# Optimization experiments

Hardware: AMD Instinct MI355X
Metric: run time of the kernel (lower is better)

Reference implementation:

```python
import jax, jax.numpy as jnp
import numpy as np

V, P, D, H, HD, L, FF = 21128, 512, 768, 12, 64, 12, 3072
COEF = np.array([[1,1,0,0,0,0,0,0,0,0,0,1],[1,1,1,1,0,0,0,0,0,0,0,1],[1,1,1,1,1,1,0,0,0,0,0,1],[1,1,1,1,1,1,1,1,0,0,0,1],[1,1,1,1,1,1,1,1,1,1,0,1]], dtype=np.float32)

def _ln(x, g, b):
    mu = jnp.mean(x, -1, keepdims=True)
    v = jnp.mean((x - mu) ** 2, -1, keepdims=True)
    return (x - mu) / jnp.sqrt(v + 1e-12) * g + b

def _gelu(x):
    return x * 0.5 * (1.0 + jax.lax.erf(x * 0.7071067811865475))

def setup_inputs() -> dict:
    key = jax.random.key(0)
    ks = jax.random.split(key, 16)
    B, S, LE = 16, 512, 256
    input_ids = jax.random.randint(ks[0], (B, S), 0, V)
    mask = jnp.ones((B, S), jnp.float32)
    epid = jax.random.randint(ks[1], (B, LE), 0, 10)
    epid = epid.at[:, -1].set(9)  # ensure encoder_turn=9 -> coefficient row 4
    s = 0.02
    def nrm(k, shape):
        return jax.random.normal(k, shape, jnp.float32) * s
    return {
        'input_ids': input_ids, 'mask': mask, 'encoder_position_id': epid,
        'word_emb': nrm(ks[2], (V, D)), 'pos_emb': nrm(ks[3], (P, D)),
        'emb_ln_g': jnp.ones((D,)), 'emb_ln_b': jnp.zeros((D,)),
        'Wq': nrm(ks[4], (L, D, D)), 'bq': jnp.zeros((L, D)),
        'Wk': nrm(ks[5], (L, D, D)), 'bk': jnp.zeros((L, D)),
        'Wv': nrm(ks[6], (L, D, D)), 'bv': jnp.zeros((L, D)),
        'Wo': nrm(ks[7], (L, D, D)), 'bo': jnp.zeros((L, D)),
        'ln1_g': jnp.ones((L, D)), 'ln1_b': jnp.zeros((L, D)),
        'Wi': nrm(ks[8], (L, D, FF)), 'bi': jnp.zeros((L, FF)),
        'Wo2': nrm(ks[9], (L, FF, D)), 'bo2': jnp.zeros((L, D)),
        'ln2_g': jnp.ones((L, D)), 'ln2_b': jnp.zeros((L, D)),
        'coef': jnp.tile(jnp.asarray(COEF)[None], (L, 1, 1)),
    }

def reference(input_ids, mask, encoder_position_id, word_emb, pos_emb, emb_ln_g, emb_ln_b,
              Wq, bq, Wk, bk, Wv, bv, Wo, bo, ln1_g, ln1_b, Wi, bi, Wo2, bo2, ln2_g, ln2_b, coef):
    B, S = input_ids.shape
    LE = encoder_position_id.shape[1]
    # causal+padding mask: floor((m+m^T)/2) on {0,1} == AND == product, then tril
    am = jnp.tril(mask[:, None, None, :] * mask[:, None, :, None])  # [B,1,S,S]
    # position coefficient machinery
    turn = jnp.max(encoder_position_id, -1)           # [B]
    row = ((turn - 1) // 2).astype(jnp.int32)         # row into [5,12] table
    enc_pm = jax.nn.one_hot(encoder_position_id, 12, dtype=jnp.float32)  # [B,LE,12]
    dec_pm = jnp.zeros((B, S - LE, 12), jnp.float32).at[:, :, 11].set(1.0)
    pm = jnp.concatenate([enc_pm, dec_pm], 1)         # [B,S,12]
    # embeddings (token_type not used in forward; past_length=0)
    h = _ln(word_emb[input_ids] + pos_emb[jnp.arange(S)], emb_ln_g, emb_ln_b)
    for l in range(L):
        coef_row = coef[l][row]                       # [B,12]
        ps = jnp.einsum('bsk,bk->bs', pm, coef_row)   # per-key modulation [B,S]
        q = (h @ Wq[l] + bq[l]).reshape(B, S, H, HD)
        k = (h @ Wk[l] + bk[l]).reshape(B, S, H, HD)
        v = (h @ Wv[l] + bv[l]).reshape(B, S, H, HD)
        scores = jnp.einsum('bqhd,bkhd->bhqk', q, k) / 8.0
        scores = scores * ps[:, None, None, :]
        scores = scores * am - 1e10 * (1.0 - am)
        probs = jax.nn.softmax(scores, -1)
        ctx = jnp.einsum('bhqk,bkhd->bqhd', probs, v).reshape(B, S, D)
        a = _ln(ctx @ Wo[l] + bo[l] + h, ln1_g[l], ln1_b[l])
        ff = _gelu(a @ Wi[l] + bi[l])
        h = _ln(ff @ Wo2[l] + bo2[l] + a, ln2_g[l], ln2_b[l])
    return h
```

## Files before the change

kernel.cpp:

```cpp
#include <hip/hip_runtime.h>

#define SEQ 512
#define NB  16
#define DIM 768
#define NH  12
#define HDIM 64
#define NL  12
#define FFD 3072
#define MTOK 8192

typedef _Float16 half8 __attribute__((ext_vector_type(8)));
typedef float    floatx4 __attribute__((ext_vector_type(4)));

__device__ __forceinline__ void load_lds16(const void* g, void* l) {
  __builtin_amdgcn_global_load_lds((__attribute__((address_space(1))) void*)g,
                                   (__attribute__((address_space(3))) void*)l, 16, 0, 0);
}

__device__ __forceinline__ float blockSum768(float v) {
  __shared__ float red[4];
  #pragma unroll
  for (int d = 32; d; d >>= 1) v += __shfl_xor(v, d);
  const int wv = threadIdx.x >> 6;
  __syncthreads();
  if ((threadIdx.x & 63) == 0) red[wv] = v;
  __syncthreads();
  return red[0] + red[1] + red[2] + red[3];
}

__device__ __forceinline__ void ln_store(float x0, float x1, float x2,
                                         const float* __restrict__ g,
                                         const float* __restrict__ bb,
                                         float* __restrict__ yf,
                                         _Float16* __restrict__ yh, int row) {
  const int tid = threadIdx.x;
  const float mu = blockSum768(x0 + x1 + x2) * (1.0f / 768.0f);
  const float d0 = x0 - mu, d1 = x1 - mu, d2 = x2 - mu;
  const float var = blockSum768(d0 * d0 + d1 * d1 + d2 * d2) * (1.0f / 768.0f);
  const float inv = rsqrtf(var + 1e-12f);
  const size_t base = (size_t)row * DIM;
  const float y0 = d0 * inv * g[tid]       + bb[tid];
  const float y1 = d1 * inv * g[tid + 256] + bb[tid + 256];
  const float y2 = d2 * inv * g[tid + 512] + bb[tid + 512];
  if (yf) { yf[base + tid] = y0; yf[base + tid + 256] = y1; yf[base + tid + 512] = y2; }
  yh[base + tid] = (_Float16)y0; yh[base + tid + 256] = (_Float16)y1; yh[base + tid + 512] = (_Float16)y2;
}

__global__ __launch_bounds__(256) void embed_ln_k(const int* __restrict__ ids,
                                                  const float* __restrict__ we,
                                                  const float* __restrict__ pe,
                                                  const float* __restrict__ g,
                                                  const float* __restrict__ bb,
                                                  float* __restrict__ hf,
                                                  _Float16* __restrict__ hh) {
  const int tok = blockIdx.x;
  const int s = tok & (SEQ - 1);
  const int id = ids[tok];
  const int tid = threadIdx.x;
  float x[3];
  #pragma unroll
  for (int j = 0; j < 3; ++j) {
    const int d = tid + j * 256;
    x[j] = we[(size_t)id * DIM + d] + pe[(size_t)s * DIM + d];
  }
  ln_store(x[0], x[1], x[2], g, bb, hf, hh, tok);
}

__global__ __launch_bounds__(256) void ln_k(const float* __restrict__ xin,
                                            const float* __restrict__ g,
                                            const float* __restrict__ bb,
                                            float* __restrict__ yf,
                                            _Float16* __restrict__ yh) {
  const int row = blockIdx.x;
  const int tid = threadIdx.x;
  float x[3];
  #pragma unroll
  for (int j = 0; j < 3; ++j) x[j] = xin[(size_t)row * DIM + tid + j * 256];
  ln_store(x[0], x[1], x[2], g, bb, yf, yh, row);
}

__global__ __launch_bounds__(256) void transpose_k(const float* __restrict__ in,
                                                   _Float16* __restrict__ out,
                                                   int K, int N) {
  __shared__ float tile[32][33];
  const int z = blockIdx.z;
  in  += (size_t)z * K * N;
  out += (size_t)z * K * N;
  const int n0 = blockIdx.x * 32, k0 = blockIdx.y * 32;
  const int tx = threadIdx.x & 31, ty = threadIdx.x >> 5;
  #pragma unroll
  for (int i = 0; i < 32; i += 8) tile[ty + i][tx] = in[(size_t)(k0 + ty + i) * N + n0 + tx];
  __syncthreads();
  #pragma unroll
  for (int i = 0; i < 32; i += 8) out[(size_t)(n0 + ty + i) * K + k0 + tx] = (_Float16)tile[tx][ty + i];
}

__global__ __launch_bounds__(512) void ps_k(const int* __restrict__ epid,
                                            const float* __restrict__ coef,
                                            float* __restrict__ ps_all) {
  __shared__ int red[8];
  const int b = blockIdx.x, tid = threadIdx.x;
  int e = (tid < 256) ? epid[b * 256 + tid] : 0;
  #pragma unroll
  for (int d = 32; d; d >>= 1) e = max(e, __shfl_xor(e, d));
  if ((tid & 63) == 0) red[tid >> 6] = e;
  __syncthreads();
  int turn = red[0];
  #pragma unroll
  for (int i = 1; i < 8; ++i) turn = max(turn, red[i]);
  int row = (turn - 1) >> 1;
  row = max(0, min(4, row));
  const int pe = (tid < 256) ? epid[b * 256 + tid] : 11;
  #pragma unroll
  for (int l = 0; l < NL; ++l)
    ps_all[((size_t)l * NB + b) * SEQ + tid] = coef[(l * 5 + row) * 12 + pe];
}

template <bool RES, bool GELU, bool WF, bool WH>
__global__ __launch_bounds__(256) void gemm_f16(const _Float16* __restrict__ A,
                                                const _Float16* __restrict__ Bt,
                                                const float* __restrict__ bias,
                                                const float* __restrict__ resid,
                                                float* __restrict__ outF,
                                                _Float16* __restrict__ outH,
                                                int M, int N, int K) {
  __shared__ __align__(16) _Float16 Als[128 * 32];
  __shared__ __align__(16) _Float16 Bls[128 * 32];
  const int tid = threadIdx.x, lane = tid & 63, wave = tid >> 6;
  const int bm0 = blockIdx.y * 128, bn0 = blockIdx.x * 128;
  const int lr = lane & 15, lk = lane >> 4;
  const int wm = (wave >> 1) * 64, wn = (wave & 1) * 64;
  floatx4 acc[4][4] = {};

  const int srow = lane >> 2;
  const int scol = (lane & 3) * 8;
  const _Float16* Ag = A  + (size_t)(bm0 + wave * 16 + srow) * K + scol;
  const _Float16* Bg = Bt + (size_t)(bn0 + wave * 16 + srow) * K + scol;
  _Float16* Al = &Als[wave * 16 * 32];
  _Float16* Bl = &Bls[wave * 16 * 32];
  const size_t rs64 = (size_t)64 * K;

  for (int kt = 0; kt < K; kt += 32) {
    load_lds16(Ag + kt,        Al);
    load_lds16(Ag + rs64 + kt, Al + 64 * 32);
    load_lds16(Bg + kt,        Bl);
    load_lds16(Bg + rs64 + kt, Bl + 64 * 32);
    __syncthreads();
    half8 af[4], bf[4];
    #pragma unroll
    for (int i = 0; i < 4; ++i) {
      af[i] = *(const half8*)&Als[(wm + i * 16 + lr) * 32 + lk * 8];
      bf[i] = *(const half8*)&Bls[(wn + i * 16 + lr) * 32 + lk * 8];
    }
    #pragma unroll
    for (int mi = 0; mi < 4; ++mi)
      #pragma unroll
      for (int ni = 0; ni < 4; ++ni)
        acc[mi][ni] = __builtin_amdgcn_mfma_f32_16x16x32_f16(af[mi], bf[ni], acc[mi][ni], 0, 0, 0);
    __syncthreads();
  }

  #pragma unroll
  for (int mi = 0; mi < 4; ++mi) {
    #pragma unroll
    for (int r = 0; r < 4; ++r) {
      const int row = bm0 + wm + mi * 16 + lk * 4 + r;
      const size_t ro = (size_t)row * N;
      #pragma unroll
      for (int ni = 0; ni < 4; ++ni) {
        const int col = bn0 + wn + ni * 16 + lr;
        float x = acc[mi][ni][r] + bias[col];
        if (RES)  x += resid[ro + col];
        if (GELU) x = 0.5f * x * (1.0f + erff(x * 0.70710678118654752f));
        if (WF) outF[ro + col] = x;
        if (WH) outH[ro + col] = (_Float16)x;
      }
    }
  }
}

__global__ __launch_bounds__(256) void attn_k(const _Float16* __restrict__ q,
                                              const _Float16* __restrict__ k,
                                              const _Float16* __restrict__ v,
                                              const float* __restrict__ ps,
                                              const float* __restrict__ mask,
                                              _Float16* __restrict__ ctx) {
  __shared__ __align__(16) _Float16 kls[64 * 64];
  __shared__ __align__(16) _Float16 vtls[64 * 64];
  __shared__ __align__(16) _Float16 pls[4][32 * 64];
  const int tid = threadIdx.x, lane = tid & 63, wave = tid >> 6;
  const int qt = blockIdx.x, h = blockIdx.y, b = blockIdx.z;
  const int lr = lane & 15, lk = lane >> 4;
  const int q0 = qt * 128 + wave * 32;

  half8 qf[2][2];
  #pragma unroll
  for (int mi = 0; mi < 2; ++mi)
    #pragma unroll
    for (int ks = 0; ks < 2; ++ks)
      qf[mi][ks] = *(const half8*)&q[(size_t)(b * SEQ + q0 + mi * 16 + lr) * DIM + h * HDIM + ks * 32 + lk * 8];

  floatx4 o[2][4] = {};
  float m_run[2][4], l_run[2][4], mq[2][4];
  #pragma unroll
  for (int mi = 0; mi < 2; ++mi)
    #pragma unroll
    for (int r = 0; r < 4; ++r) {
      m_run[mi][r] = -3e38f; l_run[mi][r] = 0.f;
      mq[mi][r] = mask[b * SEQ + q0 + mi * 16 + lk * 4 + r];
    }

  const int nt = 2 * (qt + 1);
  for (int t = 0; t < nt; ++t) {
    const int kb = t * 64;
    #pragma unroll
    for (int i = 0; i < 2; ++i) {
      const int idx = tid + i * 256;
      const int key = idx >> 3, c8 = (idx & 7) * 8;
      const size_t gkv = (size_t)(b * SEQ + kb + key) * DIM + h * HDIM + c8;
      *(half8*)&kls[key * 64 + c8] = *(const half8*)&k[gkv];
      half8 vv = *(const half8*)&v[gkv];
      #pragma unroll
      for (int j = 0; j < 8; ++j) vtls[(c8 + j) * 64 + key] = vv[j];
    }
    __syncthreads();

    floatx4 s[2][4] = {};
    #pragma unroll
    for (int ks = 0; ks < 2; ++ks)
      #pragma unroll
      for (int ni = 0; ni < 4; ++ni) {
        half8 kf = *(const half8*)&kls[(ni * 16 + lr) * 64 + ks * 32 + lk * 8];
        #pragma unroll
        for (int mi = 0; mi < 2; ++mi)
          s[mi][ni] = __builtin_amdgcn_mfma_f32_16x16x32_f16(qf[mi][ks], kf, s[mi][ni], 0, 0, 0);
      }

    float pk[4], km[4]; int kidx[4];
    #pragma unroll
    for (int ni = 0; ni < 4; ++ni) {
      kidx[ni] = kb + ni * 16 + lr;
      pk[ni] = ps[b * SEQ + kidx[ni]] * 0.125f;
      km[ni] = mask[b * SEQ + kidx[ni]];
    }

    #pragma unroll
    for (int mi = 0; mi < 2; ++mi) {
      #pragma unroll
      for (int r = 0; r < 4; ++r) {
        const int rq = q0 + mi * 16 + lk * 4 + r;
        float sc[4]; float mt = -3e38f;
        #pragma unroll
        for (int ni = 0; ni < 4; ++ni) {
          const float am = (kidx[ni] <= rq) ? km[ni] * mq[mi][r] : 0.f;
          const float x = s[mi][ni][r] * pk[ni] * am - 1e10f * (1.f - am);
          sc[ni] = x; mt = fmaxf(mt, x);
        }
        #pragma unroll
        for (int d = 1; d < 16; d <<= 1) mt = fmaxf(mt, __shfl_xor(mt, d));
        const float mnew = fmaxf(m_run[mi][r], mt);
        const float corr = __expf(m_run[mi][r] - mnew);
        float rsum = 0.f;
        #pragma unroll
        for (int ni = 0; ni < 4; ++ni) {
          const float p = __expf(sc[ni] - mnew);
          rsum += p;
          pls[wave][(mi * 16 + lk * 4 + r) * 64 + ni * 16 + lr] = (_Float16)p;
        }
        #pragma unroll
        for (int d = 1; d < 16; d <<= 1) rsum += __shfl_xor(rsum, d);
        l_run[mi][r] = l_run[mi][r] * corr + rsum;
        m_run[mi][r] = mnew;
        #pragma unroll
        for (int ni = 0; ni < 4; ++ni) o[mi][ni][r] *= corr;
      }
    }

    #pragma unroll
    for (int mi = 0; mi < 2; ++mi) {
      half8 pf[2];
      #pragma unroll
      for (int ks = 0; ks < 2; ++ks)
        pf[ks] = *(const half8*)&pls[wave][(mi * 16 + lr) * 64 + ks * 32 + lk * 8];
      #pragma unroll
      for (int ni = 0; ni < 4; ++ni)
        #pragma unroll
        for (int ks = 0; ks < 2; ++ks)
          o[mi][ni] = __builtin_amdgcn_mfma_f32_16x16x32_f16(
              pf[ks], *(const half8*)&vtls[(ni * 16 + lr) * 64 + ks * 32 + lk * 8], o[mi][ni], 0, 0, 0);
    }
    __syncthreads();
  }

  #pragma unroll
  for (int mi = 0; mi < 2; ++mi)
    #pragma unroll
    for (int r = 0; r < 4; ++r) {
      const float inv = 1.f / l_run[mi][r];
      const int rq = q0 + mi * 16 + lk * 4 + r;
      #pragma unroll
      for (int ni = 0; ni < 4; ++ni)
        ctx[(size_t)(b * SEQ + rq) * DIM + h * HDIM + ni * 16 + lr] = (_Float16)(o[mi][ni][r] * inv);
    }
}

extern "C" void kernel_launch(void* const* d_in, const int* in_sizes, int n_in,
                              void* d_out, int out_size, void* d_ws, size_t ws_size,
                              hipStream_t stream) {
  const int*   ids  = (const int*)d_in[0];
  const float* mask = (const float*)d_in[1];
  const int*   epid = (const int*)d_in[2];
  const float* we   = (const float*)d_in[3];
  const float* pe   = (const float*)d_in[4];
  const float* elng = (const float*)d_in[5];
  const float* elnb = (const float*)d_in[6];
  const float* Wq   = (const float*)d_in[7];  const float* bq  = (const float*)d_in[8];
  const float* Wk   = (const float*)d_in[9];  const float* bk  = (const float*)d_in[10];
  const float* Wv   = (const float*)d_in[11]; const float* bv  = (const float*)d_in[12];
  const float* Wo   = (const float*)d_in[13]; const float* bo  = (const float*)d_in[14];
  const float* ln1g = (const float*)d_in[15]; const float* ln1b = (const float*)d_in[16];
  const float* Wi   = (const float*)d_in[17]; const float* bi  = (const float*)d_in[18];
  const float* Wo2  = (const float*)d_in[19]; const float* bo2 = (const float*)d_in[20];
  const float* ln2g = (const float*)d_in[21]; const float* ln2b = (const float*)d_in[22];
  const float* coef = (const float*)d_in[23];
  float* out = (float*)d_out;

  char* w = (char*)d_ws;
  auto alloc = [&](size_t bytes) { char* p = w; w += (bytes + 255) & ~(size_t)255; return p; };
  const size_t WSM = (size_t)DIM * DIM;
  const size_t WLG = (size_t)DIM * FFD;
  _Float16* wqT  = (_Float16*)alloc(NL * WSM * 2);
  _Float16* wkT  = (_Float16*)alloc(NL * WSM * 2);
  _Float16* wvT  = (_Float16*)alloc(NL * WSM * 2);
  _Float16* woT  = (_Float16*)alloc(NL * WSM * 2);
  _Float16* wiT  = (_Float16*)alloc(NL * WLG * 2);
  _Float16* wo2T = (_Float16*)alloc(NL * WLG * 2);
  float*    h_f32 = (float*)alloc((size_t)MTOK * DIM * 4);
  _Float16* h_f16 = (_Float16*)alloc((size_t)MTOK * DIM * 2);
  float*    a_f32 = (float*)alloc((size_t)MTOK * DIM * 4);
  _Float16* a_f16 = (_Float16*)alloc((size_t)MTOK * DIM * 2);
  float*    tmp   = (float*)alloc((size_t)MTOK * DIM * 4);
  _Float16* q_f16 = (_Float16*)alloc((size_t)MTOK * DIM * 2);
  _Float16* k_f16 = (_Float16*)alloc((size_t)MTOK * DIM * 2);
  _Float16* v_f16 = (_Float16*)alloc((size_t)MTOK * DIM * 2);
  _Float16* c_f16 = (_Float16*)alloc((size_t)MTOK * DIM * 2);
  _Float16* ff_f16 = (_Float16*)alloc((size_t)MTOK * FFD * 2);
  float*    ps_all = (float*)alloc((size_t)NL * NB * SEQ * 4);

  transpose_k<<<dim3(24, 24, NL), 256, 0, stream>>>(Wq,  wqT,  DIM, DIM);
  transpose_k<<<dim3(24, 24, NL), 256, 0, stream>>>(Wk,  wkT,  DIM, DIM);
  transpose_k<<<dim3(24, 24, NL), 256, 0, stream>>>(Wv,  wvT,  DIM, DIM);
  transpose_k<<<dim3(24, 24, NL), 256, 0, stream>>>(Wo,  woT,  DIM, DIM);
  transpose_k<<<dim3(96, 24, NL), 256, 0, stream>>>(Wi,  wiT,  DIM, FFD);
  transpose_k<<<dim3(24, 96, NL), 256, 0, stream>>>(Wo2, wo2T, FFD, DIM);
  ps_k<<<NB, 512, 0, stream>>>(epid, coef, ps_all);
  embed_ln_k<<<MTOK, 256, 0, stream>>>(ids, we, pe, elng, elnb, h_f32, h_f16);

  for (int l = 0; l < NL; ++l) {
    gemm_f16<false, false, false, true><<<dim3(6, 64), 256, 0, stream>>>(
        h_f16, wqT + (size_t)l * WSM, bq + l * DIM, nullptr, nullptr, q_f16, MTOK, DIM, DIM);
    gemm_f16<false, false, false, true><<<dim3(6, 64), 256, 0, stream>>>(
        h_f16, wkT + (size_t)l * WSM, bk + l * DIM, nullptr, nullptr, k_f16, MTOK, DIM, DIM);
    gemm_f16<false, false, false, true><<<dim3(6, 64), 256, 0, stream>>>(
        h_f16, wvT + (size_t)l * WSM, bv + l * DIM, nullptr, nullptr, v_f16, MTOK, DIM, DIM);
    attn_k<<<dim3(4, NH, NB), 256, 0, stream>>>(
        q_f16, k_f16, v_f16, ps_all + (size_t)l * NB * SEQ, mask, c_f16);
    gemm_f16<true, false, true, false><<<dim3(6, 64), 256, 0, stream>>>(
        c_f16, woT + (size_t)l * WSM, bo + l * DIM, h_f32, tmp, nullptr, MTOK, DIM, DIM);
    ln_k<<<MTOK, 256, 0, stream>>>(tmp, ln1g + l * DIM, ln1b + l * DIM, a_f32, a_f16);
    gemm_f16<false, true, false, true><<<dim3(24, 64), 256, 0, stream>>>(
        a_f16, wiT + (size_t)l * WLG, bi + l * FFD, nullptr, nullptr, ff_f16, MTOK, FFD, DIM);
    gemm_f16<true, false, true, false><<<dim3(6, 64), 256, 0, stream>>>(
        ff_f16, wo2T + (size_t)l * WLG, bo2 + l * DIM, a_f32, tmp, nullptr, MTOK, DIM, FFD);
    ln_k<<<MTOK, 256, 0, stream>>>(tmp, ln2g + l * DIM, ln2b + l * DIM,
                                   (l == NL - 1) ? out : h_f32, h_f16);
  }
}
```

Before: 5.075 ms.

## Fuse QKV projections into one GEMM and swizzle attention LDS tiles

```diff
diff --git a/kernel.cpp b/kernel.cpp
--- a/kernel.cpp
+++ b/kernel.cpp
@@ -8,6 +8,7 @@
 #define NL  12
 #define FFD 3072
 #define MTOK 8192
+#define QKVD 2304
 
 typedef _Float16 half8 __attribute__((ext_vector_type(8)));
 typedef float    floatx4 __attribute__((ext_vector_type(4)));
@@ -81,11 +82,11 @@
 
 __global__ __launch_bounds__(256) void transpose_k(const float* __restrict__ in,
                                                    _Float16* __restrict__ out,
-                                                   int K, int N) {
+                                                   int K, int N, size_t ozs) {
   __shared__ float tile[32][33];
   const int z = blockIdx.z;
   in  += (size_t)z * K * N;
-  out += (size_t)z * K * N;
+  out += (size_t)z * ozs;
   const int n0 = blockIdx.x * 32, k0 = blockIdx.y * 32;
   const int tx = threadIdx.x & 31, ty = threadIdx.x >> 5;
   #pragma unroll
@@ -93,6 +94,18 @@
   __syncthreads();
   #pragma unroll
   for (int i = 0; i < 32; i += 8) out[(size_t)(n0 + ty + i) * K + k0 + tx] = (_Float16)tile[tx][ty + i];
+}
+
+__global__ __launch_bounds__(256) void concat_bias_k(const float* __restrict__ bq,
+                                                     const float* __restrict__ bk,
+                                                     const float* __restrict__ bv,
+                                                     float* __restrict__ dst) {
+  const int l = blockIdx.x;
+  for (int j = threadIdx.x; j < DIM; j += 256) {
+    dst[(size_t)l * QKVD + j]           = bq[l * DIM + j];
+    dst[(size_t)l * QKVD + DIM + j]     = bk[l * DIM + j];
+    dst[(size_t)l * QKVD + 2 * DIM + j] = bv[l * DIM + j];
+  }
 }
 
 __global__ __launch_bounds__(512) void ps_k(const int* __restrict__ epid,
@@ -179,9 +192,7 @@
   }
 }
 
-__global__ __launch_bounds__(256) void attn_k(const _Float16* __restrict__ q,
-                                              const _Float16* __restrict__ k,
-                                              const _Float16* __restrict__ v,
+__global__ __launch_bounds__(256) void attn_k(const _Float16* __restrict__ qkv,
                                               const float* __restrict__ ps,
                                               const float* __restrict__ mask,
                                               _Float16* __restrict__ ctx) {
@@ -189,7 +200,8 @@
   __shared__ __align__(16) _Float16 vtls[64 * 64];
   __shared__ __align__(16) _Float16 pls[4][32 * 64];
   const int tid = threadIdx.x, lane = tid & 63, wave = tid >> 6;
-  const int qt = blockIdx.x, h = blockIdx.y, b = blockIdx.z;
+  const int qt = 3 - blockIdx.x;
+  const int h = blockIdx.y, b = blockIdx.z;
   const int lr = lane & 15, lk = lane >> 4;
   const int q0 = qt * 128 + wave * 32;
 
@@ -198,7 +210,7 @@
   for (int mi = 0; mi < 2; ++mi)
     #pragma unroll
     for (int ks = 0; ks < 2; ++ks)
-      qf[mi][ks] = *(const half8*)&q[(size_t)(b * SEQ + q0 + mi * 16 + lr) * DIM + h * HDIM + ks * 32 + lk * 8];
+      qf[mi][ks] = *(const half8*)&qkv[(size_t)(b * SEQ + q0 + mi * 16 + lr) * QKVD + h * HDIM + ks * 32 + lk * 8];
 
   floatx4 o[2][4] = {};
   float m_run[2][4], l_run[2][4], mq[2][4];
@@ -210,6 +222,7 @@
       mq[mi][r] = mask[b * SEQ + q0 + mi * 16 + lk * 4 + r];
     }
 
+  const int swzA = (lr & 7) * 8;
   const int nt = 2 * (qt + 1);
   for (int t = 0; t < nt; ++t) {
     const int kb = t * 64;
@@ -217,11 +230,15 @@
     for (int i = 0; i < 2; ++i) {
       const int idx = tid + i * 256;
       const int key = idx >> 3, c8 = (idx & 7) * 8;
-      const size_t gkv = (size_t)(b * SEQ + kb + key) * DIM + h * HDIM + c8;
-      *(half8*)&kls[key * 64 + c8] = *(const half8*)&k[gkv];
-      half8 vv = *(const half8*)&v[gkv];
-      #pragma unroll
-      for (int j = 0; j < 8; ++j) vtls[(c8 + j) * 64 + key] = vv[j];
+      *(half8*)&kls[key * 64 + (c8 ^ ((key & 7) * 8))] =
+          *(const half8*)&qkv[(size_t)(b * SEQ + kb + key) * QKVD + DIM + h * HDIM + c8];
+      const int keyv = idx & 63, c8v = (idx >> 6) * 8;
+      half8 vv = *(const half8*)&qkv[(size_t)(b * SEQ + kb + keyv) * QKVD + 2 * DIM + h * HDIM + c8v];
+      #pragma unroll
+      for (int j = 0; j < 8; ++j) {
+        const int d = c8v + j;
+        vtls[d * 64 + (keyv ^ ((d & 7) * 8))] = vv[j];
+      }
     }
     __syncthreads();
 
@@ -230,7 +247,7 @@
     for (int ks = 0; ks < 2; ++ks)
       #pragma unroll
       for (int ni = 0; ni < 4; ++ni) {
-        half8 kf = *(const half8*)&kls[(ni * 16 + lr) * 64 + ks * 32 + lk * 8];
+        half8 kf = *(const half8*)&kls[(ni * 16 + lr) * 64 + ((ks * 32 + lk * 8) ^ swzA)];
         #pragma unroll
         for (int mi = 0; mi < 2; ++mi)
           s[mi][ni] = __builtin_amdgcn_mfma_f32_16x16x32_f16(qf[mi][ks], kf, s[mi][ni], 0, 0, 0);
@@ -249,6 +266,8 @@
       #pragma unroll
       for (int r = 0; r < 4; ++r) {
         const int rq = q0 + mi * 16 + lk * 4 + r;
+        const int prow = mi * 16 + lk * 4 + r;
+        const int pswz = (prow & 7) * 8;
         float sc[4]; float mt = -3e38f;
         #pragma unroll
         for (int ni = 0; ni < 4; ++ni) {
@@ -265,7 +284,7 @@
         for (int ni = 0; ni < 4; ++ni) {
           const float p = __expf(sc[ni] - mnew);
           rsum += p;
-          pls[wave][(mi * 16 + lk * 4 + r) * 64 + ni * 16 + lr] = (_Float16)p;
+          pls[wave][prow * 64 + ((ni * 16 + lr) ^ pswz)] = (_Float16)p;
         }
         #pragma unroll
         for (int d = 1; d < 16; d <<= 1) rsum += __shfl_xor(rsum, d);
@@ -281,13 +300,13 @@
       half8 pf[2];
       #pragma unroll
       for (int ks = 0; ks < 2; ++ks)
-        pf[ks] = *(const half8*)&pls[wave][(mi * 16 + lr) * 64 + ks * 32 + lk * 8];
+        pf[ks] = *(const half8*)&pls[wave][(mi * 16 + lr) * 64 + ((ks * 32 + lk * 8) ^ swzA)];
       #pragma unroll
       for (int ni = 0; ni < 4; ++ni)
         #pragma unroll
         for (int ks = 0; ks < 2; ++ks)
           o[mi][ni] = __builtin_amdgcn_mfma_f32_16x16x32_f16(
-              pf[ks], *(const half8*)&vtls[(ni * 16 + lr) * 64 + ks * 32 + lk * 8], o[mi][ni], 0, 0, 0);
+              pf[ks], *(const half8*)&vtls[(ni * 16 + lr) * 64 + ((ks * 32 + lk * 8) ^ swzA)], o[mi][ni], 0, 0, 0);
     }
     __syncthreads();
   }
@@ -329,42 +348,37 @@
   auto alloc = [&](size_t bytes) { char* p = w; w += (bytes + 255) & ~(size_t)255; return p; };
   const size_t WSM = (size_t)DIM * DIM;
   const size_t WLG = (size_t)DIM * FFD;
-  _Float16* wqT  = (_Float16*)alloc(NL * WSM * 2);
-  _Float16* wkT  = (_Float16*)alloc(NL * WSM * 2);
-  _Float16* wvT  = (_Float16*)alloc(NL * WSM * 2);
-  _Float16* woT  = (_Float16*)alloc(NL * WSM * 2);
-  _Float16* wiT  = (_Float16*)alloc(NL * WLG * 2);
-  _Float16* wo2T = (_Float16*)alloc(NL * WLG * 2);
+  _Float16* wqkvT = (_Float16*)alloc(NL * 3 * WSM * 2);
+  _Float16* woT   = (_Float16*)alloc(NL * WSM * 2);
+  _Float16* wiT   = (_Float16*)alloc(NL * WLG * 2);
+  _Float16* wo2T  = (_Float16*)alloc(NL * WLG * 2);
+  float*    bqkv  = (float*)alloc((size_t)NL * QKVD * 4);
   float*    h_f32 = (float*)alloc((size_t)MTOK * DIM * 4);
   _Float16* h_f16 = (_Float16*)alloc((size_t)MTOK * DIM * 2);
   float*    a_f32 = (float*)alloc((size_t)MTOK * DIM * 4);
   _Float16* a_f16 = (_Float16*)alloc((size_t)MTOK * DIM * 2);
   float*    tmp   = (float*)alloc((size_t)MTOK * DIM * 4);
-  _Float16* q_f16 = (_Float16*)alloc((size_t)MTOK * DIM * 2);
-  _Float16* k_f16 = (_Float16*)alloc((size_t)MTOK * DIM * 2);
-  _Float16* v_f16 = (_Float16*)alloc((size_t)MTOK * DIM * 2);
+  _Float16* qkv_f16 = (_Float16*)alloc((size_t)MTOK * QKVD * 2);
   _Float16* c_f16 = (_Float16*)alloc((size_t)MTOK * DIM * 2);
   _Float16* ff_f16 = (_Float16*)alloc((size_t)MTOK * FFD * 2);
   float*    ps_all = (float*)alloc((size_t)NL * NB * SEQ * 4);
 
-  transpose_k<<<dim3(24, 24, NL), 256, 0, stream>>>(Wq,  wqT,  DIM, DIM);
-  transpose_k<<<dim3(24, 24, NL), 256, 0, stream>>>(Wk,  wkT,  DIM, DIM);
-  transpose_k<<<dim3(24, 24, NL), 256, 0, stream>>>(Wv,  wvT,  DIM, DIM);
-  transpose_k<<<dim3(24, 24, NL), 256, 0, stream>>>(Wo,  woT,  DIM, DIM);
-  transpose_k<<<dim3(96, 24, NL), 256, 0, stream>>>(Wi,  wiT,  DIM, FFD);
-  transpose_k<<<dim3(24, 96, NL), 256, 0, stream>>>(Wo2, wo2T, FFD, DIM);
+  transpose_k<<<dim3(24, 24, NL), 256, 0, stream>>>(Wq, wqkvT,           DIM, DIM, 3 * WSM);
+  transpose_k<<<dim3(24, 24, NL), 256, 0, stream>>>(Wk, wqkvT + WSM,     DIM, DIM, 3 * WSM);
+  transpose_k<<<dim3(24, 24, NL), 256, 0, stream>>>(Wv, wqkvT + 2 * WSM, DIM, DIM, 3 * WSM);
+  transpose_k<<<dim3(24, 24, NL), 256, 0, stream>>>(Wo,  woT,  DIM, DIM, WSM);
+  transpose_k<<<dim3(96, 24, NL), 256, 0, stream>>>(Wi,  wiT,  DIM, FFD, WLG);
+  transpose_k<<<dim3(24, 96, NL), 256, 0, stream>>>(Wo2, wo2T, FFD, DIM, WLG);
+  concat_bias_k<<<NL, 256, 0, stream>>>(bq, bk, bv, bqkv);
   ps_k<<<NB, 512, 0, stream>>>(epid, coef, ps_all);
   embed_ln_k<<<MTOK, 256, 0, stream>>>(ids, we, pe, elng, elnb, h_f32, h_f16);
 
   for (int l = 0; l < NL; ++l) {
-    gemm_f16<false, false, false, true><<<dim3(6, 64), 256, 0, stream>>>(
-        h_f16, wqT + (size_t)l * WSM, bq + l * DIM, nullptr, nullptr, q_f16, MTOK, DIM, DIM);
-    gemm_f16<false, false, false, true><<<dim3(6, 64), 256, 0, stream>>>(
-        h_f16, wkT + (size_t)l * WSM, bk + l * DIM, nullptr, nullptr, k_f16, MTOK, DIM, DIM);
-    gemm_f16<false, false, false, true><<<dim3(6, 64), 256, 0, stream>>>(
-        h_f16, wvT + (size_t)l * WSM, bv + l * DIM, nullptr, nullptr, v_f16, MTOK, DIM, DIM);
+    gemm_f16<false, false, false, true><<<dim3(18, 64), 256, 0, stream>>>(
+        h_f16, wqkvT + (size_t)l * 3 * WSM, bqkv + (size_t)l * QKVD, nullptr,
+        nullptr, qkv_f16, MTOK, QKVD, DIM);
     attn_k<<<dim3(4, NH, NB), 256, 0, stream>>>(
-        q_f16, k_f16, v_f16, ps_all + (size_t)l * NB * SEQ, mask, c_f16);
+        qkv_f16, ps_all + (size_t)l * NB * SEQ, mask, c_f16);
     gemm_f16<true, false, true, false><<<dim3(6, 64), 256, 0, stream>>>(
         c_f16, woT + (size_t)l * WSM, bo + l * DIM, h_f32, tmp, nullptr, MTOK, DIM, DIM);
     ln_k<<<MTOK, 256, 0, stream>>>(tmp, ln1g + l * DIM, ln1b + l * DIM, a_f32, a_f16);
```

New measurement: 4.658 ms. 8.2% less time.
